# Kernel optimization log

Measured on AMD Instinct MI355X. Metric: run time of the kernel, lower is better.

Reference implementation:

```python
import jax, jax.numpy as jnp
import numpy as np
from jax import lax

B, S, E, V, L, H = 512, 128, 300, 100000, 2, 300


def _match_score(s1, s2, v1, v2):
    # s1,s2: [B,S,E]; v1,v2: [B,S] float valid masks (1 where token != 0)
    s1 = s1 * v1[..., None]
    s2 = s2 * v2[..., None]
    n1 = jnp.sum(s1 * s1, -1)                      # [B,S]
    n2 = jnp.sum(s2 * s2, -1)                      # [B,S]
    cross = jnp.einsum('bie,bje->bij', s1, s2)     # [B,S,S]
    d2 = n1[:, :, None] + n2[:, None, :] - 2.0 * cross
    d = jnp.sqrt(jnp.maximum(d2, 0.0))
    return 1.0 / (1.0 + d)


def _avg3(x):
    # avg_pool1d over seq dim, kernel 3, pad 1, stride 1, count_include_pad=True
    p = jnp.pad(x, ((0, 0), (1, 1), (0, 0)))
    return (p[:, :-2] + p[:, 1:-1] + p[:, 2:]) / 3.0


def _conv2d(x, w, b):
    # x: [B,2,S,E], w: [1,2,3,3], b: [1]
    y = lax.conv_general_dilated(x, w, (1, 1), ((1, 1), (1, 1)),
                                 dimension_numbers=('NCHW', 'OIHW', 'NCHW'))
    return y[:, 0] + b[0]  # squeeze out-channel -> [B,S,E]


def setup_inputs() -> dict:
    key = jax.random.key(0)
    ks = jax.random.split(key, 12)
    fc_in = E * (1 + L) * 2
    return {
        'seq1': jax.random.randint(ks[0], (B, S), 0, V),
        'seq2': jax.random.randint(ks[1], (B, S), 0, V),
        'emb': jax.random.normal(ks[2], (V, E), jnp.float32) * 0.1,
        'W': jax.random.normal(ks[3], (L, S, E), jnp.float32) * (2.0 / (S + E)) ** 0.5,
        'conv_w': jax.random.normal(ks[4], (L, 1, 2, 3, 3), jnp.float32) * 0.2,
        'conv_b': jax.random.normal(ks[5], (L, 1), jnp.float32) * 0.01,
        'fc1_w': jax.random.normal(ks[6], (H, fc_in), jnp.float32) * (1.0 / fc_in) ** 0.5,
        'fc1_b': jnp.zeros((H,), jnp.float32),
        'ln_g': jnp.ones((H,), jnp.float32),
        'ln_b': jnp.zeros((H,), jnp.float32),
        'fc2_w': jax.random.normal(ks[7], (2, H), jnp.float32) * (1.0 / H) ** 0.5,
        'fc2_b': jnp.zeros((2,), jnp.float32),
    }


def reference(seq1, seq2, emb, W, conv_w, conv_b, fc1_w, fc1_b, ln_g, ln_b, fc2_w, fc2_b):
    v1 = (seq1 != 0).astype(jnp.float32)
    v2 = (seq2 != 0).astype(jnp.float32)
    s1 = emb[seq1]  # [B,S,E]
    s2 = emb[seq2]
    res1, res2 = [s1.mean(1)], [s2.mean(1)]
    for i in range(L):
        A = _match_score(s1, s2, v1, v2)                 # [B,S,S]
        f1 = jnp.einsum('bij,je->bie', A, W[i])
        f2 = jnp.einsum('bji,je->bie', A, W[i])          # A^T @ W
        o1 = jnp.tanh(_conv2d(jnp.stack([s1, f1], 1), conv_w[i], conv_b[i]))
        o2 = jnp.tanh(_conv2d(jnp.stack([s2, f2], 1), conv_w[i], conv_b[i]))
        res1.append(o1.mean(1))
        res2.append(o2.mean(1))
        A2 = _match_score(o1, o2, v1, v2)
        w1 = A2.sum(-1)                                   # [B,S]
        w2 = A2.sum(1)
        p1 = _avg3(o1 * w1[..., None])
        p2 = _avg3(o2 * w2[..., None])
        s1, s2 = p1 + s1, p2 + s2
    x = jnp.concatenate([jnp.concatenate(res1, 1), jnp.concatenate(res2, 1)], 1)
    h = x @ fc1_w.T + fc1_b
    mu = h.mean(-1, keepdims=True)
    var = ((h - mu) ** 2).mean(-1, keepdims=True)
    h = (h - mu) * lax.rsqrt(var + 1e-5) * ln_g + ln_b
    h = jax.nn.relu(h)
    out = h @ fc2_w.T + fc2_b
    prob = jax.nn.softmax(out, axis=-1)
    return out, prob
```

## Files before the change

kernel.cpp:

```cpp
#include <hip/hip_runtime.h>
#include <math.h>

#define BB 512
#define SS 128
#define EE 300
#define HH 300
#define FCIN 1800
#define LLI 2
#define KP 320

using half8 = __attribute__((ext_vector_type(8))) _Float16;
using h2    = __attribute__((ext_vector_type(2))) _Float16;
using f32x4 = __attribute__((ext_vector_type(4))) float;

__device__ __forceinline__ float fast_tanh(float x){
    float ax = fabsf(x);
    float t = __expf(-2.f*ax);
    float r = (1.f - t) / (1.f + t);
    return copysignf(r, x);
}

__device__ __forceinline__ float norm8(half8 hv, float n){
    h2 p0 = __builtin_shufflevector(hv, hv, 0, 1);
    h2 p1 = __builtin_shufflevector(hv, hv, 2, 3);
    h2 p2 = __builtin_shufflevector(hv, hv, 4, 5);
    h2 p3 = __builtin_shufflevector(hv, hv, 6, 7);
    n = __builtin_amdgcn_fdot2(p0, p0, n, false);
    n = __builtin_amdgcn_fdot2(p1, p1, n, false);
    n = __builtin_amdgcn_fdot2(p2, p2, n, false);
    n = __builtin_amdgcn_fdot2(p3, p3, n, false);
    return n;
}

__global__ void wt_build_kernel(const float* __restrict__ W, _Float16* __restrict__ Wt){
    int idx = blockIdx.x*256 + threadIdx.x;
    if (idx >= 2*KP*SS) return;
    int j = idx & 127;
    int e = (idx >> 7) % KP;
    int it = idx / (KP*SS);
    float v = (e < EE) ? W[(size_t)it*SS*EE + j*EE + e] : 0.f;
    Wt[idx] = (_Float16)v;
}

__global__ void cwpack_kernel(const float* __restrict__ cw, const float* __restrict__ cb,
                              float* __restrict__ pwt){
    int t = threadIdx.x;
    if (t < 12){
        int it = t / 6, rem = t % 6;
        const float* w = cw + it*18 + rem*3;
        float a = w[0], b = w[1], d = w[2];
        h2 p01 = { (_Float16)a, (_Float16)b };
        h2 p12 = { (_Float16)b, (_Float16)d };
        float* o = pwt + it*32;
        ((unsigned*)o)[rem]   = __builtin_bit_cast(unsigned, p01);
        ((unsigned*)o)[6+rem] = __builtin_bit_cast(unsigned, p12);
        o[12+rem] = a;
        o[18+rem] = d;
    }
    if (t < 2) pwt[t*32+24] = cb[t];
}

__global__ __launch_bounds__(256) void embed_kernel(
    const int* __restrict__ seq1, const int* __restrict__ seq2,
    const float* __restrict__ emb,
    _Float16* __restrict__ sf1, _Float16* __restrict__ sf2,
    float* __restrict__ v1, float* __restrict__ v2,
    float* __restrict__ res, int b0){
    __shared__ float mred[4][320];
    int bl = blockIdx.x, which = blockIdx.z;
    int w = threadIdx.x >> 6;
    int r = blockIdx.y*4 + w;
    int l = threadIdx.x & 63;
    const int* seq = which ? seq2 : seq1;
    _Float16* sfg = (which ? sf2 : sf1) + (size_t)bl*SS*KP;
    float* vd = (which ? v2 : v1) + bl*SS;
    int token = seq[(size_t)(b0+bl)*SS + r];
    if (l == 0) vd[r] = (token != 0) ? 1.f : 0.f;
    const float* er = emb + (size_t)token * EE;
    int e0 = l*8;
    float x[8];
    if (l < 37){
        float4 a = *(const float4*)(er + e0);
        float4 b = *(const float4*)(er + e0 + 4);
        x[0]=a.x; x[1]=a.y; x[2]=a.z; x[3]=a.w;
        x[4]=b.x; x[5]=b.y; x[6]=b.z; x[7]=b.w;
    } else if (l == 37){
        x[0]=er[296]; x[1]=er[297]; x[2]=er[298]; x[3]=er[299];
        x[4]=0.f; x[5]=0.f; x[6]=0.f; x[7]=0.f;
    } else {
        #pragma unroll
        for (int j = 0; j < 8; j++) x[j] = 0.f;
    }
    if (l < 40){
        half8 hv;
        #pragma unroll
        for (int j = 0; j < 8; j++) hv[j] = (_Float16)x[j];
        *(half8*)(sfg + r*KP + e0) = hv;
        #pragma unroll
        for (int j = 0; j < 8; j++) mred[w][e0 + j] = x[j];
    }
    __syncthreads();
    for (int e = threadIdx.x; e < EE; e += 256){
        float s = mred[0][e] + mred[1][e] + mred[2][e] + mred[3][e];
        atomicAdd(&res[(size_t)(b0+bl)*FCIN + which*900 + e], s * (1.f/SS));
    }
}

__global__ __launch_bounds__(320) void mean16_kernel(
    const _Float16* __restrict__ src1, const _Float16* __restrict__ src2,
    float* __restrict__ res, int b0, int seg){
    int bl = blockIdx.x, which = blockIdx.y;
    const _Float16* src = (which ? src2 : src1) + (size_t)bl*SS*KP;
    int e = threadIdx.x;
    if (e >= EE) return;
    float acc = 0.f;
    #pragma unroll 4
    for (int r = 0; r < SS; r++) acc += (float)src[r*KP + e];
    res[(size_t)(b0+bl)*FCIN + which*900 + seg*300 + e] = acc * (1.f/SS);
}

__global__ __launch_bounds__(512, 4) void cross_matchA(
    const _Float16* __restrict__ sfA, const _Float16* __restrict__ sfB,
    const float* __restrict__ vAg, const float* __restrict__ vBg,
    _Float16* __restrict__ Ab16)
{
    __shared__ _Float16 As[128][40];
    __shared__ _Float16 Bs[128][40];
    __shared__ float nAl[128], nBl[128], vAl[128], vBl[128];

    int bl = blockIdx.x;
    int tid = threadIdx.x;
    int w = tid >> 6, lane = tid & 63;
    int m = lane & 15, quad = lane >> 4;

    const _Float16* gA = sfA + (size_t)bl*SS*KP;
    const _Float16* gB = sfB + (size_t)bl*SS*KP;

    if (tid < 128){ vAl[tid] = vAg[bl*SS + tid]; }
    else if (tid < 256){ vBl[tid-128] = vBg[bl*SS + tid-128]; }

    f32x4 acc[8];
    #pragma unroll
    for (int c = 0; c < 8; c++) acc[c] = (f32x4){0.f,0.f,0.f,0.f};

    int srow = tid >> 2, skq = (tid & 3) * 8;
    int arow = w*16 + m;
    float nA = 0.f, nB = 0.f;

    for (int kc = 0; kc < 10; kc++){
        __syncthreads();
        {
            half8 ha = *(const half8*)(gA + srow*KP + kc*32 + skq);
            half8 hb = *(const half8*)(gB + srow*KP + kc*32 + skq);
            ha = ha * (_Float16)vAl[srow];
            hb = hb * (_Float16)vBl[srow];
            *(half8*)&As[srow][skq] = ha;
            *(half8*)&Bs[srow][skq] = hb;
            nA = norm8(ha, nA);
            nB = norm8(hb, nB);
        }
        __syncthreads();
        half8 a = *(const half8*)&As[arow][quad*8];
        #pragma unroll
        for (int c = 0; c < 8; c++){
            half8 b = *(const half8*)&Bs[c*16 + m][quad*8];
            acc[c] = __builtin_amdgcn_mfma_f32_16x16x32_f16(a, b, acc[c], 0, 0, 0);
        }
    }

    nA += __shfl_xor(nA, 1); nA += __shfl_xor(nA, 2);
    nB += __shfl_xor(nB, 1); nB += __shfl_xor(nB, 2);
    if ((tid & 3) == 0){ nAl[srow] = nA; nBl[srow] = nB; }
    __syncthreads();

    int ibase = w*16 + quad*4;
    _Float16* Ao = Ab16 + (size_t)bl*SS*SS;
    #pragma unroll
    for (int c = 0; c < 8; c++){
        int j = c*16 + m;
        float nc = nBl[j];
        #pragma unroll
        for (int r = 0; r < 4; r++){
            int i = ibase + r;
            float d2 = nAl[i] + nc - 2.f*acc[c][r];
            float d = sqrtf(fmaxf(d2, 0.f));
            Ao[i*SS + j] = (_Float16)(1.f / (1.f + d));
        }
    }
}

__global__ __launch_bounds__(512, 4) void cross_sums_pool(
    const _Float16* __restrict__ oA, const _Float16* __restrict__ oB,
    const float* __restrict__ vAg, const float* __restrict__ vBg,
    _Float16* __restrict__ sf1, _Float16* __restrict__ sf2)
{
    __shared__ _Float16 As[128][40];
    __shared__ _Float16 Bs[128][40];
    __shared__ float nAl[128], nBl[128], vAl[128], vBl[128];
    __shared__ float colred[8][132];
    __shared__ float wr[128], wc[128];

    int bl = blockIdx.x;
    int tid = threadIdx.x;
    int w = tid >> 6, lane = tid & 63;
    int m = lane & 15, quad = lane >> 4;

    const _Float16* gA = oA + (size_t)bl*SS*KP;
    const _Float16* gB = oB + (size_t)bl*SS*KP;

    if (tid < 128){ vAl[tid] = vAg[bl*SS + tid]; }
    else if (tid < 256){ vBl[tid-128] = vBg[bl*SS + tid-128]; }

    f32x4 acc[8];
    #pragma unroll
    for (int c = 0; c < 8; c++) acc[c] = (f32x4){0.f,0.f,0.f,0.f};

    int srow = tid >> 2, skq = (tid & 3) * 8;
    int arow = w*16 + m;
    float nA = 0.f, nB = 0.f;

    for (int kc = 0; kc < 10; kc++){
        __syncthreads();
        {
            half8 ha = *(const half8*)(gA + srow*KP + kc*32 + skq);
            half8 hb = *(const half8*)(gB + srow*KP + kc*32 + skq);
            ha = ha * (_Float16)vAl[srow];
            hb = hb * (_Float16)vBl[srow];
            *(half8*)&As[srow][skq] = ha;
            *(half8*)&Bs[srow][skq] = hb;
            nA = norm8(ha, nA);
            nB = norm8(hb, nB);
        }
        __syncthreads();
        half8 a = *(const half8*)&As[arow][quad*8];
        #pragma unroll
        for (int c = 0; c < 8; c++){
            half8 b = *(const half8*)&Bs[c*16 + m][quad*8];
            acc[c] = __builtin_amdgcn_mfma_f32_16x16x32_f16(a, b, acc[c], 0, 0, 0);
        }
    }

    nA += __shfl_xor(nA, 1); nA += __shfl_xor(nA, 2);
    nB += __shfl_xor(nB, 1); nB += __shfl_xor(nB, 2);
    if ((tid & 3) == 0){ nAl[srow] = nA; nBl[srow] = nB; }
    __syncthreads();

    int ibase = w*16 + quad*4;
    float aval[8][4];
    #pragma unroll
    for (int c = 0; c < 8; c++){
        float nc = nBl[c*16 + m];
        #pragma unroll
        for (int r = 0; r < 4; r++){
            float d2 = nAl[ibase+r] + nc - 2.f*acc[c][r];
            float d = sqrtf(fmaxf(d2, 0.f));
            aval[c][r] = 1.f / (1.f + d);
        }
    }

    float rp[4];
    #pragma unroll
    for (int r = 0; r < 4; r++){
        float s = 0.f;
        #pragma unroll
        for (int c = 0; c < 8; c++) s += aval[c][r];
        rp[r] = s;
    }
    #pragma unroll
    for (int mask = 1; mask < 16; mask <<= 1)
        #pragma unroll
        for (int r = 0; r < 4; r++) rp[r] += __shfl_xor(rp[r], mask);
    if (m == 0){
        #pragma unroll
        for (int r = 0; r < 4; r++) wr[ibase + r] = rp[r];
    }
    float cp[8];
    #pragma unroll
    for (int c = 0; c < 8; c++){
        float s = 0.f;
        #pragma unroll
        for (int r = 0; r < 4; r++) s += aval[c][r];
        cp[c] = s;
    }
    #pragma unroll
    for (int c = 0; c < 8; c++){
        cp[c] += __shfl_xor(cp[c], 16);
        cp[c] += __shfl_xor(cp[c], 32);
    }
    if (quad == 0){
        #pragma unroll
        for (int c = 0; c < 8; c++) colred[w][c*16 + m] = cp[c];
    }
    __syncthreads();
    if (tid < 128){
        float s = 0.f;
        #pragma unroll
        for (int g = 0; g < 8; g++) s += colred[g][tid];
        wc[tid] = s;
    }
    __syncthreads();

    int prow = tid >> 2, sub = tid & 3;
    #pragma unroll
    for (int which = 0; which < 2; which++){
        const _Float16* og = which ? gB : gA;
        const float* wv = which ? wc : wr;
        _Float16* sg = (which ? sf2 : sf1) + (size_t)bl*SS*KP;
        float w0 = wv[prow];
        float wm = (prow > 0)   ? wv[prow-1] : 0.f;
        float wp = (prow < 127) ? wv[prow+1] : 0.f;
        #pragma unroll
        for (int k = 0; k < 10; k++){
            int e0 = (sub + k*4) * 8;
            half8 o0 = *(const half8*)(og + prow*KP + e0);
            half8 om = {};
            half8 op = {};
            if (prow > 0)   om = *(const half8*)(og + (prow-1)*KP + e0);
            if (prow < 127) op = *(const half8*)(og + (prow+1)*KP + e0);
            half8 sv = *(const half8*)(sg + prow*KP + e0);
            half8 outh;
            #pragma unroll
            for (int j = 0; j < 8; j++){
                float a = (float)o0[j]*w0 + (float)om[j]*wm + (float)op[j]*wp;
                float ns = (float)sv[j] + a * (1.f/3.f);
                outh[j] = (_Float16)ns;
            }
            *(half8*)(sg + prow*KP + e0) = outh;
        }
    }
}

__global__ __launch_bounds__(256, 4) void f_conv_kernel(
    const _Float16* __restrict__ Ab, const _Float16* __restrict__ Wt,
    const _Float16* __restrict__ sf1, const _Float16* __restrict__ sf2,
    const float* __restrict__ pw,
    _Float16* __restrict__ o16_1, _Float16* __restrict__ o16_2)
{
    __shared__ _Float16 Atile[128][136];
    _Float16 (*ftile)[104] = (_Float16(*)[104])&Atile[0][0];

    int bl = blockIdx.x, es = blockIdx.y, zz = blockIdx.z;
    int C0 = es*80;
    int tid = threadIdx.x, w = tid >> 6, lane = tid & 63;
    int m = lane & 15, quad = lane >> 4;

    const unsigned* pu = (const unsigned*)pw;
    h2 w01[2][3], w12[2][3];
    float w0f[2][3], w2f[2][3];
    #pragma unroll
    for (int c = 0; c < 2; c++)
        #pragma unroll
        for (int dy = 0; dy < 3; dy++){
            int rem = c*3 + dy;
            w01[c][dy] = __builtin_bit_cast(h2, pu[rem]);
            w12[c][dy] = __builtin_bit_cast(h2, pu[6 + rem]);
            w0f[c][dy] = pw[12 + rem];
            w2f[c][dy] = pw[18 + rem];
        }
    float bias = pw[24];

    const _Float16* gA = Ab + (size_t)bl*SS*SS;
    if (zz == 0){
        #pragma unroll
        for (int u = 0; u < 8; u++){
            int idx = tid + u*256;
            int row = idx >> 4, jc = (idx & 15)*8;
            *(float4*)&Atile[row][jc] = *(const float4*)(gA + row*SS + jc);
        }
    } else {
        #pragma unroll
        for (int u = 0; u < 8; u++){
            int idx = tid + u*256;
            int row = idx >> 4, jc = (idx & 15)*8;
            half8 hv = *(const half8*)(gA + row*SS + jc);
            #pragma unroll
            for (int j = 0; j < 8; j++) Atile[jc+j][row] = hv[j];
        }
    }
    __syncthreads();

    f32x4 acc[2][6];
    #pragma unroll
    for (int f = 0; f < 2; f++)
        #pragma unroll
        for (int c = 0; c < 6; c++) acc[f][c] = (f32x4){0.f,0.f,0.f,0.f};
    #pragma unroll
    for (int kc = 0; kc < 4; kc++){
        half8 a0 = *(const half8*)&Atile[w*32 + m][kc*32 + quad*8];
        half8 a1 = *(const half8*)&Atile[w*32 + 16 + m][kc*32 + quad*8];
        #pragma unroll
        for (int c = 0; c < 6; c++){
            int e = C0 - 8 + c*16 + m;
            half8 b = *(const half8*)(Wt + (ptrdiff_t)e*SS + kc*32 + quad*8);
            acc[0][c] = __builtin_amdgcn_mfma_f32_16x16x32_f16(a0, b, acc[0][c], 0, 0, 0);
            acc[1][c] = __builtin_amdgcn_mfma_f32_16x16x32_f16(a1, b, acc[1][c], 0, 0, 0);
        }
    }
    __syncthreads();

    #pragma unroll
    for (int f = 0; f < 2; f++)
        #pragma unroll
        for (int c = 0; c < 6; c++){
            int e = C0 - 8 + c*16 + m;
            int lc = c*16 + m;
            bool ev = (e >= 0) && (e < EE);
            #pragma unroll
            for (int r = 0; r < 4; r++){
                int i = w*32 + f*16 + quad*4 + r;
                ftile[i][lc] = ev ? (_Float16)acc[f][c][r] : (_Float16)0.f;
            }
        }
    __syncthreads();

    int rr = tid >> 1, half = tid & 1;
    int cb = C0 + half*40;
    const _Float16* cs = (zz ? sf2 : sf1) + (size_t)bl*SS*KP;
    _Float16* od = (zz ? o16_2 : o16_1) + (size_t)bl*SS*KP;
    int lc0 = half*40 + 8;

    float cacc[5][8];
    #pragma unroll
    for (int k = 0; k < 5; k++)
        #pragma unroll
        for (int j = 0; j < 8; j++) cacc[k][j] = bias;

    #pragma unroll
    for (int c = 0; c < 2; c++){
        #pragma unroll
        for (int dy = 0; dy < 3; dy++){
            int gr = rr + dy - 1;
            bool rok = (gr >= 0) && (gr < SS);
            half8 d[5];
            float L = 0.f, R = 0.f;
            #pragma unroll
            for (int k = 0; k < 5; k++) d[k] = (half8){};
            if (rok){
                if (c == 0){
                    #pragma unroll
                    for (int k = 0; k < 5; k++)
                        d[k] = *(const half8*)(cs + gr*KP + cb + k*8);
                    if (cb > 0)       L = (float)cs[gr*KP + cb - 1];
                    if (cb + 40 < KP) R = (float)cs[gr*KP + cb + 40];
                } else {
                    #pragma unroll
                    for (int k = 0; k < 5; k++)
                        d[k] = *(const half8*)&ftile[gr][lc0 + k*8];
                    L = (float)ftile[gr][lc0 - 1];
                    R = (float)ftile[gr][lc0 + 40];
                }
            }
            h2 W01 = w01[c][dy], W12 = w12[c][dy];
            float W0 = w0f[c][dy], W2 = w2f[c][dy];
            #pragma unroll
            for (int k = 0; k < 5; k++){
                float xm = (k == 0) ? L : (float)d[k-1][7];
                float xp = (k == 4) ? R : (float)d[k+1][0];
                h2 p0 = __builtin_shufflevector(d[k], d[k], 0, 1);
                h2 p1 = __builtin_shufflevector(d[k], d[k], 2, 3);
                h2 p2 = __builtin_shufflevector(d[k], d[k], 4, 5);
                h2 p3 = __builtin_shufflevector(d[k], d[k], 6, 7);
                cacc[k][0] = __builtin_amdgcn_fdot2(W12, p0, cacc[k][0], false);
                cacc[k][0] = fmaf(W0, xm, cacc[k][0]);
                cacc[k][1] = __builtin_amdgcn_fdot2(W01, p0, cacc[k][1], false);
                cacc[k][1] = fmaf(W2, (float)d[k][2], cacc[k][1]);
                cacc[k][2] = __builtin_amdgcn_fdot2(W12, p1, cacc[k][2], false);
                cacc[k][2] = fmaf(W0, (float)d[k][1], cacc[k][2]);
                cacc[k][3] = __builtin_amdgcn_fdot2(W01, p1, cacc[k][3], false);
                cacc[k][3] = fmaf(W2, (float)d[k][4], cacc[k][3]);
                cacc[k][4] = __builtin_amdgcn_fdot2(W12, p2, cacc[k][4], false);
                cacc[k][4] = fmaf(W0, (float)d[k][3], cacc[k][4]);
                cacc[k][5] = __builtin_amdgcn_fdot2(W01, p2, cacc[k][5], false);
                cacc[k][5] = fmaf(W2, (float)d[k][6], cacc[k][5]);
                cacc[k][6] = __builtin_amdgcn_fdot2(W12, p3, cacc[k][6], false);
                cacc[k][6] = fmaf(W0, (float)d[k][5], cacc[k][6]);
                cacc[k][7] = __builtin_amdgcn_fdot2(W01, p3, cacc[k][7], false);
                cacc[k][7] = fmaf(W2, xp, cacc[k][7]);
            }
        }
    }

    #pragma unroll
    for (int k = 0; k < 5; k++){
        half8 outh;
        #pragma unroll
        for (int j = 0; j < 8; j++){
            int e = cb + k*8 + j;
            float t = (e < EE) ? fast_tanh(cacc[k][j]) : 0.f;
            outh[j] = (_Float16)t;
        }
        *(half8*)(od + rr*KP + cb + k*8) = outh;
    }
}

#define CKK 12
__global__ __launch_bounds__(256) void fc1_kernel(const float* __restrict__ res,
                                                  const float* __restrict__ fw,
                                                  float* __restrict__ h){
    __shared__ float Xt[CKK][68];
    __shared__ float Wts[CKK][68];
    int bt = blockIdx.x, jt = blockIdx.y, kz = blockIdx.z;
    int tid = threadIdx.x, tx = tid & 15, ty = tid >> 4;
    int b0l = bt*64, j0 = jt*64, kbase = kz*300;
    float acc[4][4] = {};
    for (int k0 = 0; k0 < 300; k0 += CKK){
        #pragma unroll
        for (int u = 0; u < 3; u++){
            int idx = tid + u*256;
            int a = idx / CKK, k = idx - a*CKK;
            Xt[k][a] = res[(size_t)(b0l+a)*FCIN + kbase + k0 + k];
            int gj = j0 + a;
            Wts[k][a] = (gj < HH) ? fw[(size_t)gj*FCIN + kbase + k0 + k] : 0.f;
        }
        __syncthreads();
        #pragma unroll
        for (int k = 0; k < CKK; k++){
            float xv[4], wv[4];
            #pragma unroll
            for (int r = 0; r < 4; r++) xv[r] = Xt[k][ty*4+r];
            #pragma unroll
            for (int c = 0; c < 4; c++) wv[c] = Wts[k][tx*4+c];
            #pragma unroll
            for (int r = 0; r < 4; r++)
                #pragma unroll
                for (int c = 0; c < 4; c++)
                    acc[r][c] = fmaf(xv[r], wv[c], acc[r][c]);
        }
        __syncthreads();
    }
    #pragma unroll
    for (int r = 0; r < 4; r++){
        int gb = b0l + ty*4 + r;
        #pragma unroll
        for (int c = 0; c < 4; c++){
            int gj = j0 + tx*4 + c;
            if (gj < HH) atomicAdd(&h[(size_t)gb*HH + gj], acc[r][c]);
        }
    }
}

__global__ void head_kernel(const float* __restrict__ h, const float* __restrict__ fb,
                            const float* __restrict__ g,
                            const float* __restrict__ be, const float* __restrict__ f2w,
                            const float* __restrict__ f2b, float* __restrict__ out){
    int b = blockIdx.x, tid = threadIdx.x;
    __shared__ float arr[HH];
    __shared__ float s_s[4], s_q[4], r0[4], r1[4];
    float x0 = (tid < HH) ? h[(size_t)b*HH + tid] + fb[tid] : 0.f;
    float x1 = (tid + 256 < HH) ? h[(size_t)b*HH + tid + 256] + fb[tid+256] : 0.f;
    float s = x0 + x1, sq = x0*x0 + x1*x1;
    #pragma unroll
    for (int o = 32; o > 0; o >>= 1){ s += __shfl_down(s, o); sq += __shfl_down(sq, o); }
    int wv = tid >> 6, ln = tid & 63;
    if (ln == 0){ s_s[wv] = s; s_q[wv] = sq; }
    __syncthreads();
    s  = s_s[0] + s_s[1] + s_s[2] + s_s[3];
    sq = s_q[0] + s_q[1] + s_q[2] + s_q[3];
    float mean = s / HH;
    float var = sq / HH - mean*mean;
    float inv = rsqrtf(var + 1e-5f);
    if (tid < HH)       arr[tid]     = fmaxf((x0 - mean)*inv*g[tid]     + be[tid],     0.f);
    if (tid + 256 < HH) arr[tid+256] = fmaxf((x1 - mean)*inv*g[tid+256] + be[tid+256], 0.f);
    __syncthreads();
    float p0 = 0.f, p1 = 0.f;
    for (int j = tid; j < HH; j += 256){ float hv = arr[j]; p0 += hv*f2w[j]; p1 += hv*f2w[HH+j]; }
    #pragma unroll
    for (int o = 32; o > 0; o >>= 1){ p0 += __shfl_down(p0, o); p1 += __shfl_down(p1, o); }
    if (ln == 0){ r0[wv] = p0; r1[wv] = p1; }
    __syncthreads();
    if (tid == 0){
        float o0 = r0[0]+r0[1]+r0[2]+r0[3] + f2b[0];
        float o1 = r1[0]+r1[1]+r1[2]+r1[3] + f2b[1];
        out[b*2+0] = o0; out[b*2+1] = o1;
        float m = fmaxf(o0, o1);
        float e0 = __expf(o0 - m), e1 = __expf(o1 - m);
        float den = e0 + e1;
        out[BB*2 + b*2+0] = e0/den;
        out[BB*2 + b*2+1] = e1/den;
    }
}

extern "C" void kernel_launch(void* const* d_in, const int* in_sizes, int n_in,
                              void* d_out, int out_size, void* d_ws, size_t ws_size,
                              hipStream_t stream){
    const int*   seq1   = (const int*)d_in[0];
    const int*   seq2   = (const int*)d_in[1];
    const float* emb    = (const float*)d_in[2];
    const float* W      = (const float*)d_in[3];
    const float* conv_w = (const float*)d_in[4];
    const float* conv_b = (const float*)d_in[5];
    const float* fc1_w  = (const float*)d_in[6];
    const float* fc1_b  = (const float*)d_in[7];
    const float* ln_g   = (const float*)d_in[8];
    const float* ln_b   = (const float*)d_in[9];
    const float* fc2_w  = (const float*)d_in[10];
    const float* fc2_b  = (const float*)d_in[11];
    float* out = (float*)d_out;

    float* ws = (float*)d_ws;
    size_t fixedf = (size_t)BB*FCIN + (size_t)BB*HH + (size_t)KP*SS + 64;
    size_t perb = (size_t)2*SS*KP + (size_t)(SS*SS/2) + 2*SS;
    size_t avail = ws_size / 4;
    long long bcl = (long long)((avail > fixedf ? avail - fixedf : 0) / perb);
    int BC = (int)(bcl < 1 ? 1 : (bcl > BB ? BB : bcl));

    float* res = ws;
    float* hb  = res + (size_t)BB*FCIN;
    _Float16* Wt = (_Float16*)(hb + (size_t)BB*HH);
    float* pwt = (float*)(Wt + (size_t)2*KP*SS);
    _Float16* sf1 = (_Float16*)(pwt + 64);
    _Float16* sf2 = sf1 + (size_t)BC*SS*KP;
    _Float16* o16_1 = sf2 + (size_t)BC*SS*KP;
    _Float16* o16_2 = o16_1 + (size_t)BC*SS*KP;
    _Float16* Ab  = o16_2 + (size_t)BC*SS*KP;
    float* v1  = (float*)(Ab + (size_t)BC*SS*SS);
    float* v2  = v1 + (size_t)BC*SS;

    wt_build_kernel<<<(2*KP*SS + 255)/256, 256, 0, stream>>>(W, Wt);
    cwpack_kernel<<<1, 64, 0, stream>>>(conv_w, conv_b, pwt);
    hipMemsetAsync(hb, 0, (size_t)BB*HH*sizeof(float), stream);
    hipMemsetAsync(res, 0, (size_t)BB*FCIN*sizeof(float), stream);

    for (int b0 = 0; b0 < BB; b0 += BC){
        int bc = (BB - b0 < BC) ? (BB - b0) : BC;
        embed_kernel<<<dim3(bc, 32, 2), 256, 0, stream>>>(seq1, seq2, emb, sf1, sf2,
                                                          v1, v2, res, b0);
        for (int it = 0; it < LLI; it++){
            cross_matchA<<<bc, 512, 0, stream>>>(sf1, sf2, v1, v2, Ab);
            f_conv_kernel<<<dim3(bc, 4, 2), 256, 0, stream>>>(Ab, Wt + (size_t)it*KP*SS,
                                                              sf1, sf2, pwt + it*32,
                                                              o16_1, o16_2);
            mean16_kernel<<<dim3(bc, 2), 320, 0, stream>>>(o16_1, o16_2, res, b0, it+1);
            cross_sums_pool<<<bc, 512, 0, stream>>>(o16_1, o16_2, v1, v2, sf1, sf2);
        }
    }
    fc1_kernel<<<dim3(8, 5, 6), 256, 0, stream>>>(res, fc1_w, hb);
    head_kernel<<<BB, 256, 0, stream>>>(hb, fc1_b, ln_g, ln_b, fc2_w, fc2_b, out);
}
```

Before: 795.7 us.

## Write transposed match matrix and compute full-width f tile per block in f_conv

cross_matchA now also writes a transposed copy of the match score matrix, so f_conv no longer transposes A through shared memory. f_conv is restructured from 4 column slices per batch to one 512-thread block per batch and side. Each block computes all 304 padded columns of A·W into a swizzled 80KB shared tile and then runs the conv over the full width. This removes the redundant A tile loads, halo recomputation and extra launches, at the cost of extra global writes for AbT, a larger workspace per batch (smaller chunk size), lower occupancy from the big shared tile, and strided uncoalesced transposed stores.

```diff
diff --git a/kernel.cpp b/kernel.cpp
--- a/kernel.cpp
+++ b/kernel.cpp
@@ -30,6 +30,12 @@
     n = __builtin_amdgcn_fdot2(p2, p2, n, false);
     n = __builtin_amdgcn_fdot2(p3, p3, n, false);
     return n;
+}
+
+__device__ __forceinline__ int fswz(int row, int col){
+    int ch = col >> 3;
+    int chs = (ch & ~7) | ((ch ^ row) & 7);
+    return row*320 + chs*8 + (col & 7);
 }
 
 __global__ void wt_build_kernel(const float* __restrict__ W, _Float16* __restrict__ Wt){
@@ -122,7 +128,7 @@
 __global__ __launch_bounds__(512, 4) void cross_matchA(
     const _Float16* __restrict__ sfA, const _Float16* __restrict__ sfB,
     const float* __restrict__ vAg, const float* __restrict__ vBg,
-    _Float16* __restrict__ Ab16)
+    _Float16* __restrict__ Ab16, _Float16* __restrict__ AbT16)
 {
     __shared__ _Float16 As[128][40];
     __shared__ _Float16 Bs[128][40];
@@ -175,6 +181,7 @@
 
     int ibase = w*16 + quad*4;
     _Float16* Ao = Ab16 + (size_t)bl*SS*SS;
+    _Float16* AoT = AbT16 + (size_t)bl*SS*SS;
     #pragma unroll
     for (int c = 0; c < 8; c++){
         int j = c*16 + m;
@@ -184,7 +191,9 @@
             int i = ibase + r;
             float d2 = nAl[i] + nc - 2.f*acc[c][r];
             float d = sqrtf(fmaxf(d2, 0.f));
-            Ao[i*SS + j] = (_Float16)(1.f / (1.f + d));
+            _Float16 val = (_Float16)(1.f / (1.f + d));
+            Ao[i*SS + j] = val;
+            AoT[j*SS + i] = val;
         }
     }
 }
@@ -330,17 +339,16 @@
     }
 }
 
-__global__ __launch_bounds__(256, 4) void f_conv_kernel(
-    const _Float16* __restrict__ Ab, const _Float16* __restrict__ Wt,
+__global__ __launch_bounds__(512, 4) void f_conv_kernel(
+    const _Float16* __restrict__ Ab, const _Float16* __restrict__ AbT,
+    const _Float16* __restrict__ Wt,
     const _Float16* __restrict__ sf1, const _Float16* __restrict__ sf2,
     const float* __restrict__ pw,
     _Float16* __restrict__ o16_1, _Float16* __restrict__ o16_2)
 {
-    __shared__ _Float16 Atile[128][136];
-    _Float16 (*ftile)[104] = (_Float16(*)[104])&Atile[0][0];
-
-    int bl = blockIdx.x, es = blockIdx.y, zz = blockIdx.z;
-    int C0 = es*80;
+    __shared__ _Float16 ftile[128*320];
+
+    int bl = blockIdx.x, zz = blockIdx.y;
     int tid = threadIdx.x, w = tid >> 6, lane = tid & 63;
     int m = lane & 15, quad = lane >> 4;
 
@@ -359,137 +367,115 @@
         }
     float bias = pw[24];
 
-    const _Float16* gA = Ab + (size_t)bl*SS*SS;
-    if (zz == 0){
-        #pragma unroll
-        for (int u = 0; u < 8; u++){
-            int idx = tid + u*256;
-            int row = idx >> 4, jc = (idx & 15)*8;
-            *(float4*)&Atile[row][jc] = *(const float4*)(gA + row*SS + jc);
-        }
-    } else {
-        #pragma unroll
-        for (int u = 0; u < 8; u++){
-            int idx = tid + u*256;
-            int row = idx >> 4, jc = (idx & 15)*8;
-            half8 hv = *(const half8*)(gA + row*SS + jc);
-            #pragma unroll
-            for (int j = 0; j < 8; j++) Atile[jc+j][row] = hv[j];
-        }
-    }
-    __syncthreads();
-
-    f32x4 acc[2][6];
-    #pragma unroll
-    for (int f = 0; f < 2; f++)
-        #pragma unroll
-        for (int c = 0; c < 6; c++) acc[f][c] = (f32x4){0.f,0.f,0.f,0.f};
-    #pragma unroll
-    for (int kc = 0; kc < 4; kc++){
-        half8 a0 = *(const half8*)&Atile[w*32 + m][kc*32 + quad*8];
-        half8 a1 = *(const half8*)&Atile[w*32 + 16 + m][kc*32 + quad*8];
-        #pragma unroll
-        for (int c = 0; c < 6; c++){
-            int e = C0 - 8 + c*16 + m;
-            half8 b = *(const half8*)(Wt + (ptrdiff_t)e*SS + kc*32 + quad*8);
-            acc[0][c] = __builtin_amdgcn_mfma_f32_16x16x32_f16(a0, b, acc[0][c], 0, 0, 0);
-            acc[1][c] = __builtin_amdgcn_mfma_f32_16x16x32_f16(a1, b, acc[1][c], 0, 0, 0);
-        }
-    }
-    __syncthreads();
-
-    #pragma unroll
-    for (int f = 0; f < 2; f++)
-        #pragma unroll
-        for (int c = 0; c < 6; c++){
-            int e = C0 - 8 + c*16 + m;
-            int lc = c*16 + m;
-            bool ev = (e >= 0) && (e < EE);
-            #pragma unroll
-            for (int r = 0; r < 4; r++){
-                int i = w*32 + f*16 + quad*4 + r;
-                ftile[i][lc] = ev ? (_Float16)acc[f][c][r] : (_Float16)0.f;
-            }
-        }
-    __syncthreads();
-
-    int rr = tid >> 1, half = tid & 1;
-    int cb = C0 + half*40;
+    const _Float16* gA = (zz ? AbT : Ab) + (size_t)bl*SS*SS;
+    int arow = w*16 + m;
+    half8 a[4];
+    #pragma unroll
+    for (int kc = 0; kc < 4; kc++)
+        a[kc] = *(const half8*)(gA + arow*SS + kc*32 + quad*8);
+
+    #pragma unroll
+    for (int c = 0; c < 19; c++){
+        int e = c*16 + m;
+        f32x4 acc = (f32x4){0.f,0.f,0.f,0.f};
+        #pragma unroll
+        for (int kc = 0; kc < 4; kc++){
+            half8 b = *(const half8*)(Wt + (size_t)e*SS + kc*32 + quad*8);
+            acc = __builtin_amdgcn_mfma_f32_16x16x32_f16(a[kc], b, acc, 0, 0, 0);
+        }
+        bool ev = (e < EE);
+        #pragma unroll
+        for (int r = 0; r < 4; r++){
+            int i = w*16 + quad*4 + r;
+            ftile[fswz(i, e)] = ev ? (_Float16)acc[r] : (_Float16)0.f;
+        }
+    }
+    {
+        int zr = tid >> 2, zc0 = 304 + (tid & 3)*4;
+        #pragma unroll
+        for (int j = 0; j < 4; j++) ftile[fswz(zr, zc0 + j)] = (_Float16)0.f;
+    }
+    __syncthreads();
+
+    int rr = tid >> 2, seg = tid & 3;
     const _Float16* cs = (zz ? sf2 : sf1) + (size_t)bl*SS*KP;
     _Float16* od = (zz ? o16_2 : o16_1) + (size_t)bl*SS*KP;
-    int lc0 = half*40 + 8;
-
-    float cacc[5][8];
-    #pragma unroll
-    for (int k = 0; k < 5; k++)
-        #pragma unroll
-        for (int j = 0; j < 8; j++) cacc[k][j] = bias;
-
-    #pragma unroll
-    for (int c = 0; c < 2; c++){
-        #pragma unroll
-        for (int dy = 0; dy < 3; dy++){
-            int gr = rr + dy - 1;
-            bool rok = (gr >= 0) && (gr < SS);
-            half8 d[5];
-            float L = 0.f, R = 0.f;
+
+    #pragma unroll
+    for (int p = 0; p < 2; p++){
+        int cb = seg*80 + p*40;
+        float cacc[5][8];
+        #pragma unroll
+        for (int k = 0; k < 5; k++)
             #pragma unroll
-            for (int k = 0; k < 5; k++) d[k] = (half8){};
-            if (rok){
-                if (c == 0){
-                    #pragma unroll
-                    for (int k = 0; k < 5; k++)
-                        d[k] = *(const half8*)(cs + gr*KP + cb + k*8);
-                    if (cb > 0)       L = (float)cs[gr*KP + cb - 1];
-                    if (cb + 40 < KP) R = (float)cs[gr*KP + cb + 40];
-                } else {
-                    #pragma unroll
-                    for (int k = 0; k < 5; k++)
-                        d[k] = *(const half8*)&ftile[gr][lc0 + k*8];
-                    L = (float)ftile[gr][lc0 - 1];
-                    R = (float)ftile[gr][lc0 + 40];
+            for (int j = 0; j < 8; j++) cacc[k][j] = bias;
+
+        #pragma unroll
+        for (int c = 0; c < 2; c++){
+            #pragma unroll
+            for (int dy = 0; dy < 3; dy++){
+                int gr = rr + dy - 1;
+                bool rok = (gr >= 0) && (gr < SS);
+                half8 d[5];
+                float L = 0.f, R = 0.f;
+                #pragma unroll
+                for (int k = 0; k < 5; k++) d[k] = (half8){};
+                if (rok){
+                    if (c == 0){
+                        #pragma unroll
+                        for (int k = 0; k < 5; k++)
+                            d[k] = *(const half8*)(cs + gr*KP + cb + k*8);
+                        if (cb > 0)       L = (float)cs[gr*KP + cb - 1];
+                        if (cb + 40 < KP) R = (float)cs[gr*KP + cb + 40];
+                    } else {
+                        #pragma unroll
+                        for (int k = 0; k < 5; k++)
+                            d[k] = *(const half8*)&ftile[fswz(gr, cb + k*8)];
+                        if (cb > 0)        L = (float)ftile[fswz(gr, cb - 1)];
+                        if (cb + 40 < 320) R = (float)ftile[fswz(gr, cb + 40)];
+                    }
+                }
+                h2 W01 = w01[c][dy], W12 = w12[c][dy];
+                float W0 = w0f[c][dy], W2 = w2f[c][dy];
+                #pragma unroll
+                for (int k = 0; k < 5; k++){
+                    float xm = (k == 0) ? L : (float)d[k-1][7];
+                    float xp = (k == 4) ? R : (float)d[k+1][0];
+                    h2 p0 = __builtin_shufflevector(d[k], d[k], 0, 1);
+                    h2 p1 = __builtin_shufflevector(d[k], d[k], 2, 3);
+                    h2 p2 = __builtin_shufflevector(d[k], d[k], 4, 5);
+                    h2 p3 = __builtin_shufflevector(d[k], d[k], 6, 7);
+                    cacc[k][0] = __builtin_amdgcn_fdot2(W12, p0, cacc[k][0], false);
+                    cacc[k][0] = fmaf(W0, xm, cacc[k][0]);
+                    cacc[k][1] = __builtin_amdgcn_fdot2(W01, p0, cacc[k][1], false);
+                    cacc[k][1] = fmaf(W2, (float)d[k][2], cacc[k][1]);
+                    cacc[k][2] = __builtin_amdgcn_fdot2(W12, p1, cacc[k][2], false);
+                    cacc[k][2] = fmaf(W0, (float)d[k][1], cacc[k][2]);
+                    cacc[k][3] = __builtin_amdgcn_fdot2(W01, p1, cacc[k][3], false);
+                    cacc[k][3] = fmaf(W2, (float)d[k][4], cacc[k][3]);
+                    cacc[k][4] = __builtin_amdgcn_fdot2(W12, p2, cacc[k][4], false);
+                    cacc[k][4] = fmaf(W0, (float)d[k][3], cacc[k][4]);
+                    cacc[k][5] = __builtin_amdgcn_fdot2(W01, p2, cacc[k][5], false);
+                    cacc[k][5] = fmaf(W2, (float)d[k][6], cacc[k][5]);
+                    cacc[k][6] = __builtin_amdgcn_fdot2(W12, p3, cacc[k][6], false);
+                    cacc[k][6] = fmaf(W0, (float)d[k][5], cacc[k][6]);
+                    cacc[k][7] = __builtin_amdgcn_fdot2(W01, p3, cacc[k][7], false);
+                    cacc[k][7] = fmaf(W2, xp, cacc[k][7]);
                 }
             }
-            h2 W01 = w01[c][dy], W12 = w12[c][dy];
-            float W0 = w0f[c][dy], W2 = w2f[c][dy];
+        }
+
+        #pragma unroll
+        for (int k = 0; k < 5; k++){
+            half8 outh;
             #pragma unroll
-            for (int k = 0; k < 5; k++){
-                float xm = (k == 0) ? L : (float)d[k-1][7];
-                float xp = (k == 4) ? R : (float)d[k+1][0];
-                h2 p0 = __builtin_shufflevector(d[k], d[k], 0, 1);
-                h2 p1 = __builtin_shufflevector(d[k], d[k], 2, 3);
-                h2 p2 = __builtin_shufflevector(d[k], d[k], 4, 5);
-                h2 p3 = __builtin_shufflevector(d[k], d[k], 6, 7);
-                cacc[k][0] = __builtin_amdgcn_fdot2(W12, p0, cacc[k][0], false);
-                cacc[k][0] = fmaf(W0, xm, cacc[k][0]);
-                cacc[k][1] = __builtin_amdgcn_fdot2(W01, p0, cacc[k][1], false);
-                cacc[k][1] = fmaf(W2, (float)d[k][2], cacc[k][1]);
-                cacc[k][2] = __builtin_amdgcn_fdot2(W12, p1, cacc[k][2], false);
-                cacc[k][2] = fmaf(W0, (float)d[k][1], cacc[k][2]);
-                cacc[k][3] = __builtin_amdgcn_fdot2(W01, p1, cacc[k][3], false);
-                cacc[k][3] = fmaf(W2, (float)d[k][4], cacc[k][3]);
-                cacc[k][4] = __builtin_amdgcn_fdot2(W12, p2, cacc[k][4], false);
-                cacc[k][4] = fmaf(W0, (float)d[k][3], cacc[k][4]);
-                cacc[k][5] = __builtin_amdgcn_fdot2(W01, p2, cacc[k][5], false);
-                cacc[k][5] = fmaf(W2, (float)d[k][6], cacc[k][5]);
-                cacc[k][6] = __builtin_amdgcn_fdot2(W12, p3, cacc[k][6], false);
-                cacc[k][6] = fmaf(W0, (float)d[k][5], cacc[k][6]);
-                cacc[k][7] = __builtin_amdgcn_fdot2(W01, p3, cacc[k][7], false);
-                cacc[k][7] = fmaf(W2, xp, cacc[k][7]);
+            for (int j = 0; j < 8; j++){
+                int e = cb + k*8 + j;
+                float t = (e < EE) ? fast_tanh(cacc[k][j]) : 0.f;
+                outh[j] = (_Float16)t;
             }
-        }
-    }
-
-    #pragma unroll
-    for (int k = 0; k < 5; k++){
-        half8 outh;
-        #pragma unroll
-        for (int j = 0; j < 8; j++){
-            int e = cb + k*8 + j;
-            float t = (e < EE) ? fast_tanh(cacc[k][j]) : 0.f;
-            outh[j] = (_Float16)t;
-        }
-        *(half8*)(od + rr*KP + cb + k*8) = outh;
+            *(half8*)(od + rr*KP + cb + k*8) = outh;
+        }
     }
 }
 
@@ -599,7 +585,7 @@
 
     float* ws = (float*)d_ws;
     size_t fixedf = (size_t)BB*FCIN + (size_t)BB*HH + (size_t)KP*SS + 64;
-    size_t perb = (size_t)2*SS*KP + (size_t)(SS*SS/2) + 2*SS;
+    size_t perb = (size_t)2*SS*KP + (size_t)(SS*SS) + 2*SS;
     size_t avail = ws_size / 4;
     long long bcl = (long long)((avail > fixedf ? avail - fixedf : 0) / perb);
     int BC = (int)(bcl < 1 ? 1 : (bcl > BB ? BB : bcl));
@@ -613,7 +599,8 @@
     _Float16* o16_1 = sf2 + (size_t)BC*SS*KP;
     _Float16* o16_2 = o16_1 + (size_t)BC*SS*KP;
     _Float16* Ab  = o16_2 + (size_t)BC*SS*KP;
-    float* v1  = (float*)(Ab + (size_t)BC*SS*SS);
+    _Float16* AbT = Ab + (size_t)BC*SS*SS;
+    float* v1  = (float*)(AbT + (size_t)BC*SS*SS);
     float* v2  = v1 + (size_t)BC*SS;
 
     wt_build_kernel<<<(2*KP*SS + 255)/256, 256, 0, stream>>>(W, Wt);
@@ -626,10 +613,10 @@
         embed_kernel<<<dim3(bc, 32, 2), 256, 0, stream>>>(seq1, seq2, emb, sf1, sf2,
                                                           v1, v2, res, b0);
         for (int it = 0; it < LLI; it++){
-            cross_matchA<<<bc, 512, 0, stream>>>(sf1, sf2, v1, v2, Ab);
-            f_conv_kernel<<<dim3(bc, 4, 2), 256, 0, stream>>>(Ab, Wt + (size_t)it*KP*SS,
-                                                              sf1, sf2, pwt + it*32,
-                                                              o16_1, o16_2);
+            cross_matchA<<<bc, 512, 0, stream>>>(sf1, sf2, v1, v2, Ab, AbT);
+            f_conv_kernel<<<dim3(bc, 2), 512, 0, stream>>>(Ab, AbT, Wt + (size_t)it*KP*SS,
+                                                           sf1, sf2, pwt + it*32,
+                                                           o16_1, o16_2);
             mean16_kernel<<<dim3(bc, 2), 320, 0, stream>>>(o16_1, o16_2, res, b0, it+1);
             cross_sums_pool<<<bc, 512, 0, stream>>>(o16_1, o16_2, v1, v2, sf1, sf2);
         }
```

Result: slower. 912.1 us (+14.6%).
